# Kernel optimization log

Measured on AMD Instinct MI355X. Metric: run time of the kernel, lower is better.

Reference implementation:

```python
import jax, jax.numpy as jnp
import numpy as np

N = 50000          # nodes
E = 800000         # edges (before self-loops)
F_IN, F_HID, F_OUT = 128, 64, 64
NEG_SLOPE_ATT = 0.2   # GATConv internal leaky_relu
NEG_SLOPE_ACT = 0.01  # F.leaky_relu default between layers


def setup_inputs() -> dict:
    key = jax.random.key(0)
    ks = jax.random.split(key, 16)

    def glorot(k, shape):
        fan = float(sum(shape)) if len(shape) > 1 else float(shape[0])
        return jax.random.normal(k, shape, jnp.float32) * (2.0 / fan) ** 0.5

    return {
        "x": jax.random.normal(ks[0], (N, F_IN), jnp.float32),
        "edge_index": jax.random.randint(ks[1], (2, E), 0, N, dtype=jnp.int64),
        "W1": glorot(ks[2], (F_IN, F_HID)),
        "a_src1": glorot(ks[3], (F_HID,)),
        "a_dst1": glorot(ks[4], (F_HID,)),
        "b1": jnp.zeros((F_HID,), jnp.float32),
        "W2": glorot(ks[5], (F_HID, F_HID)),
        "a_src2": glorot(ks[6], (F_HID,)),
        "a_dst2": glorot(ks[7], (F_HID,)),
        "b2": jnp.zeros((F_HID,), jnp.float32),
        "W3": glorot(ks[8], (F_HID, F_OUT)),
        "a_src3": glorot(ks[9], (F_OUT,)),
        "a_dst3": glorot(ks[10], (F_OUT,)),
        "b3": jnp.zeros((F_OUT,), jnp.float32),
    }


def gat_conv(h, src, dst, W, a_src, a_dst, b):
    # Single-head PyG GATConv: project, per-edge scores, segment softmax over dst, scatter-add.
    z = h @ W                              # [N, C]
    e_src = z @ a_src                      # [N]
    e_dst = z @ a_dst                      # [N]
    e = jax.nn.leaky_relu(e_src[src] + e_dst[dst], NEG_SLOPE_ATT)  # [E']
    m = jax.ops.segment_max(e, dst, num_segments=N)
    ex = jnp.exp(e - m[dst])
    denom = jax.ops.segment_sum(ex, dst, num_segments=N)
    alpha = ex / (denom[dst] + 1e-16)      # segment softmax (PyG adds 1e-16)
    out = jax.ops.segment_sum(alpha[:, None] * z[src], dst, num_segments=N) + b
    return out, alpha


def reference(x, edge_index, W1, a_src1, a_dst1, b1, W2, a_src2, a_dst2, b2, W3, a_src3, a_dst3, b3):
    # add_self_loops=True (GATConv default): append (i, i) for every node
    loops = jnp.arange(N, dtype=edge_index.dtype)
    ei = jnp.concatenate([edge_index, jnp.stack([loops, loops])], axis=1)  # [2, E+N]
    src, dst = ei[0], ei[1]

    h = x
    alpha = None
    for (W, asr, ads, b) in ((W1, a_src1, a_dst1, b1),
                             (W2, a_src2, a_dst2, b2),
                             (W3, a_src3, a_dst3, b3)):
        h, alpha = gat_conv(h, src, dst, W, asr, ads, b)
        h = jax.nn.leaky_relu(h, NEG_SLOPE_ACT)
    return (h, ei, alpha)
```

## Files before the change

kernel.cpp:

```cpp
#include <hip/hip_runtime.h>
#include <hip/hip_bf16.h>
#include <hip/hip_fp8.h>

#define NN 50000
#define EE 800000
#define E2 850000
#define F_IN 128
#define F_HID 64
#define NTILE  ((NN + 63) / 64)
#define AGGB 2048

#define PNB 32
#define BCAP 32768
#define HBCH 512
#define CBB2 ((EE + HBCH - 1) / HBCH)
#define HCAP 40
#define SLICEB 64
#define BSPAN 1563

__device__ __forceinline__ unsigned char f32_to_fp8(float x) {
    __hip_fp8_e4m3 t(x);
    return t.__x;
}
__device__ __forceinline__ float fp8_to_f32(unsigned char b) {
    __hip_fp8_e4m3 t; t.__x = b;
    return (float)t;
}

#if defined(__has_builtin)
#  if __has_builtin(__builtin_amdgcn_cvt_f32_fp8)
#    define CVT_FP8(v, s) __builtin_amdgcn_cvt_f32_fp8((v), (s))
#  endif
#endif
#ifndef CVT_FP8
#  define CVT_FP8(v, s) fp8_to_f32(((v) >> (8 * (s))) & 255)
#endif

__global__ __launch_bounds__(256) void cast_bin(const int* __restrict__ ei,
                                                int* __restrict__ bin_cur,
                                                unsigned long long* __restrict__ bins,
                                                float* __restrict__ ei_out) {
    __shared__ unsigned long long buf[PNB * HCAP];
    __shared__ int wcnt[4][PNB];
    __shared__ int woff[4][PNB];
    __shared__ int tcn[PNB];
    __shared__ int gbase[PNB];
    __shared__ int pfx[PNB + 1];

    int tid = threadIdx.x, wv = tid >> 6;
    if (tid < 4 * PNB) ((int*)wcnt)[tid] = 0;
    __syncthreads();

    int e0 = blockIdx.x * HBCH;
    int nE = EE - e0; if (nE > HBCH) nE = HBCH;

    int sR[2], dR[2], bR[2], rk[2];
    bool act[2];
#pragma unroll
    for (int it = 0; it < 2; ++it) {
        int idx = it * 256 + tid;
        bool a = idx < nE;
        act[it] = a;
        int e = e0 + idx;
        int ss = 0, dd = 0, bb = 0, r = 0;
        if (a) {
            ss = ei[e]; dd = ei[EE + e];
            ei_out[e]      = (float)ss;
            ei_out[E2 + e] = (float)dd;
            bb = (int)(((long long)dd * PNB) / NN);
            r = atomicAdd(&wcnt[wv][bb], 1);
        }
        sR[it] = ss; dR[it] = dd; bR[it] = bb; rk[it] = r;
    }
    __syncthreads();

    if (tid < PNB) {
        int b = tid, r = 0;
        for (int w2 = 0; w2 < 4; ++w2) { int c = wcnt[w2][b]; woff[w2][b] = r; r += c; }
        int cl = (r > HCAP) ? HCAP : r;
        tcn[b] = cl;
        gbase[b] = cl ? atomicAdd(&bin_cur[b], cl) : 0;
    }
    __syncthreads();
    if (tid == 0) {
        int run = 0;
        for (int b = 0; b < PNB; ++b) { pfx[b] = run; run += tcn[b]; }
        pfx[PNB] = run;
    }
    __syncthreads();

#pragma unroll
    for (int it = 0; it < 2; ++it) {
        if (act[it]) {
            int b = bR[it];
            int idx = woff[wv][b] + rk[it];
            unsigned long long pk =
                ((unsigned long long)(unsigned)dR[it] << 32) | (unsigned)sR[it];
            if (idx < HCAP) buf[b * HCAP + idx] = pk;
            else {
                int p = atomicAdd(&bin_cur[b], 1);
                if (p < BCAP) bins[(size_t)b * BCAP + p] = pk;
            }
        }
    }
    __syncthreads();

    int total = pfx[PNB];
    for (int idx = tid; idx < total; idx += 256) {
        int lo = 0, hi = PNB;
        while (hi - lo > 1) { int mid = (lo + hi) >> 1; if (pfx[mid] <= idx) lo = mid; else hi = mid; }
        int b = lo, li = idx - pfx[b];
        int p = gbase[b] + li;
        if (p < BCAP) bins[(size_t)b * BCAP + p] = buf[b * HCAP + li];
    }
}

__global__ __launch_bounds__(1024) void count_scan(const int* __restrict__ bin_cur,
                                                   const unsigned long long* __restrict__ bins,
                                                   int* __restrict__ deg,
                                                   int* __restrict__ offs,
                                                   int* __restrict__ cursor,
                                                   int* __restrict__ src_sorted,
                                                   float* __restrict__ ei_out,
                                                   int* __restrict__ ticket,
                                                   int* __restrict__ flag,
                                                   int* __restrict__ bsum,
                                                   int* __restrict__ bbase) {
    __shared__ int cnt[BSPAN];
    __shared__ int wsm[16];
    __shared__ int totsh, lastsh, basesh;
    int t = threadIdx.x, lane = t & 63, wid = t >> 6;
    int b = blockIdx.x;
    int lo = (int)(((long long)b * NN + PNB - 1) / PNB);
    int hi = (int)(((long long)(b + 1) * NN + PNB - 1) / PNB);
    if (hi > NN) hi = NN;
    int span = hi - lo;
    for (int i = t; i < span; i += 1024) cnt[i] = 0;
    __syncthreads();
    int n = bin_cur[b]; if (n > BCAP) n = BCAP;
    const unsigned long long* bp = bins + (size_t)b * BCAP;
    for (int i = t; i < n; i += 1024)
        atomicAdd(&cnt[(int)(bp[i] >> 32) - lo], 1);
    __syncthreads();

    int i0 = 2 * t, i1 = 2 * t + 1;
    int v0 = (i0 < span) ? cnt[i0] + 1 : 0;
    int v1 = (i1 < span) ? cnt[i1] + 1 : 0;
    int s = v0 + v1, inc = s;
#pragma unroll
    for (int dd = 1; dd < 64; dd <<= 1) {
        int o = __shfl_up(inc, dd);
        if (lane >= dd) inc += o;
    }
    if (lane == 63) wsm[wid] = inc;
    __syncthreads();
    if (t < 16) {
        int v = wsm[t], ii = v;
#pragma unroll
        for (int dd = 1; dd < 16; dd <<= 1) {
            int o = __shfl_up(ii, dd);
            if (t >= dd) ii += o;
        }
        wsm[t] = ii - v;
        if (t == 15) totsh = ii;
    }
    __syncthreads();
    int eth = wsm[wid] + (inc - s);

    if (t == 0) {
        atomicExch(&bsum[b], totsh);
        __threadfence();
        lastsh = (atomicAdd(ticket, 1) == PNB - 1) ? 1 : 0;
    }
    __syncthreads();
    if (lastsh) {
        if (t == 0) {
            int run = 0;
            for (int q = 0; q < PNB; ++q) {
                int v = atomicAdd(&bsum[q], 0);
                atomicExch(&bbase[q], run);
                run += v;
            }
            __threadfence();
            atomicExch(flag, 1);
        }
    } else {
        if (t == 0) {
            while (atomicAdd(flag, 0) == 0) __builtin_amdgcn_s_sleep(8);
        }
    }
    __syncthreads();
    if (t == 0) basesh = atomicAdd(&bbase[b], 0);
    __syncthreads();
    int base = basesh;

    if (i0 < span) {
        int d = lo + i0, ex = base + eth;
        offs[d] = ex; cursor[d] = ex + 1; deg[d] = v0 - 1;
        src_sorted[ex] = d;
        ei_out[EE + d]      = (float)d;
        ei_out[E2 + EE + d] = (float)d;
    }
    if (i1 < span) {
        int d = lo + i1, ex = base + eth + v0;
        offs[d] = ex; cursor[d] = ex + 1; deg[d] = v1 - 1;
        src_sorted[ex] = d;
        ei_out[EE + d]      = (float)d;
        ei_out[E2 + EE + d] = (float)d;
    }
}

__global__ __launch_bounds__(256) void scatter_bins(const int* __restrict__ bin_cur,
                                                    const unsigned long long* __restrict__ bins,
                                                    int* __restrict__ cursor,
                                                    int* __restrict__ src_sorted) {
    int b = blockIdx.x & (PNB - 1);
    int slice = blockIdx.x >> 5;
    int cnt = bin_cur[b];
    if (cnt > BCAP) cnt = BCAP;
    const unsigned long long* bp = bins + (size_t)b * BCAP;
    for (int i = slice * 256 + threadIdx.x; i < cnt; i += SLICEB * 256) {
        unsigned long long v = bp[i];
        int d = (int)(v >> 32);
        int s = (int)(v & 0xffffffffu);
        int pos = atomicAdd(&cursor[d], 1);
        src_sorted[pos] = s;
    }
}

template <int K>
__global__ __launch_bounds__(256) void gemm_tile(const float* __restrict__ h,
                                                 const float* __restrict__ W,
                                                 const float* __restrict__ a_src,
                                                 const float* __restrict__ a_dst,
                                                 unsigned char* __restrict__ z8,
                                                 float* __restrict__ es,
                                                 float* __restrict__ ed) {
    constexpr int LDA = K + 4;
    __shared__ float Alds[64 * LDA];
    __shared__ float Blds[K * 64];

    int tid = threadIdx.x;
    int base = blockIdx.x * 64;

    {
        constexpr int F4R = K / 4;
        for (int t = tid; t < 64 * F4R; t += 256) {
            int r = t / F4R;
            int c4 = t % F4R;
            int gr = base + r;
            if (gr >= NN) gr = NN - 1;
            float4 v = *(const float4*)(h + (size_t)gr * K + c4 * 4);
            *(float4*)(&Alds[r * LDA + c4 * 4]) = v;
        }
    }
    for (int t = tid; t < K * 16; t += 256) {
        float4 v = *(const float4*)(W + t * 4);
        *(float4*)(&Blds[t * 4]) = v;
    }
    __syncthreads();

    int tx = tid & 15;
    int ty = tid >> 4;

    float acc[4][4] = {};
#pragma unroll 4
    for (int k = 0; k < K; k += 4) {
        float4 a[4], b[4];
#pragma unroll
        for (int i = 0; i < 4; ++i)
            a[i] = *(const float4*)(&Alds[(4 * ty + i) * LDA + k]);
#pragma unroll
        for (int kk = 0; kk < 4; ++kk)
            b[kk] = *(const float4*)(&Blds[(k + kk) * 64 + 4 * tx]);
#pragma unroll
        for (int i = 0; i < 4; ++i) {
            acc[i][0] = fmaf(a[i].x, b[0].x, acc[i][0]);
            acc[i][1] = fmaf(a[i].x, b[0].y, acc[i][1]);
            acc[i][2] = fmaf(a[i].x, b[0].z, acc[i][2]);
            acc[i][3] = fmaf(a[i].x, b[0].w, acc[i][3]);
            acc[i][0] = fmaf(a[i].y, b[1].x, acc[i][0]);
            acc[i][1] = fmaf(a[i].y, b[1].y, acc[i][1]);
            acc[i][2] = fmaf(a[i].y, b[1].z, acc[i][2]);
            acc[i][3] = fmaf(a[i].y, b[1].w, acc[i][3]);
            acc[i][0] = fmaf(a[i].z, b[2].x, acc[i][0]);
            acc[i][1] = fmaf(a[i].z, b[2].y, acc[i][1]);
            acc[i][2] = fmaf(a[i].z, b[2].z, acc[i][2]);
            acc[i][3] = fmaf(a[i].z, b[2].w, acc[i][3]);
            acc[i][0] = fmaf(a[i].w, b[3].x, acc[i][0]);
            acc[i][1] = fmaf(a[i].w, b[3].y, acc[i][1]);
            acc[i][2] = fmaf(a[i].w, b[3].z, acc[i][2]);
            acc[i][3] = fmaf(a[i].w, b[3].w, acc[i][3]);
        }
    }

    float4 as4 = *(const float4*)(a_src + 4 * tx);
    float4 ad4 = *(const float4*)(a_dst + 4 * tx);
    float ps[4], pd[4];
#pragma unroll
    for (int i = 0; i < 4; ++i) {
        int gr = base + 4 * ty + i;
        if (gr < NN) {
            unsigned int pk = (unsigned int)f32_to_fp8(acc[i][0])
                            | ((unsigned int)f32_to_fp8(acc[i][1]) << 8)
                            | ((unsigned int)f32_to_fp8(acc[i][2]) << 16)
                            | ((unsigned int)f32_to_fp8(acc[i][3]) << 24);
            *(unsigned int*)(&z8[(size_t)gr * 64 + 4 * tx]) = pk;
        }
        ps[i] = acc[i][0] * as4.x + acc[i][1] * as4.y + acc[i][2] * as4.z + acc[i][3] * as4.w;
        pd[i] = acc[i][0] * ad4.x + acc[i][1] * ad4.y + acc[i][2] * ad4.z + acc[i][3] * ad4.w;
    }
#pragma unroll
    for (int d = 1; d < 16; d <<= 1) {
#pragma unroll
        for (int i = 0; i < 4; ++i) {
            ps[i] += __shfl_xor(ps[i], d);
            pd[i] += __shfl_xor(pd[i], d);
        }
    }
    if (tx == 0) {
#pragma unroll
        for (int i = 0; i < 4; ++i) {
            int gr = base + 4 * ty + i;
            if (gr < NN) { es[gr] = ps[i]; ed[gr] = pd[i]; }
        }
    }
}

__global__ __launch_bounds__(256) void aggregate(const int* __restrict__ offs,
                                                 const int* __restrict__ deg,
                                                 const int* __restrict__ src_sorted,
                                                 const float* __restrict__ es,
                                                 const float* __restrict__ ed,
                                                 const unsigned char* __restrict__ z8,
                                                 const float* __restrict__ bias,
                                                 float* __restrict__ hout,
                                                 float* __restrict__ denom_out) {
    __shared__ unsigned long long swl[4][64];
    int tid = threadIdx.x;
    int lane = tid & 63;
    int wslot = tid >> 6;
    int wave = blockIdx.x * 4 + wslot;
    const int NW = AGGB * 4;

    int sub  = lane >> 4;
    int fgrp = (lane & 15) * 4;
    const unsigned char* zp = z8 + fgrp;
    float4 bi4 = *(const float4*)(bias + fgrp);

    int n = wave;
    if (n >= NN) return;
    n = __builtin_amdgcn_readfirstlane(n);
    int off = offs[n];
    int dg = deg[n] + 1;
    float edn = ed[n];
    int sv = src_sorted[off + ((lane < dg) ? lane : 0)];
    float ese = es[sv];

    while (true) {
        int n2 = n + NW;
        bool more = (n2 < NN);
        int off2 = 0, dg2 = 0; float edn2 = 0.f;
        if (more) {
            n2 = __builtin_amdgcn_readfirstlane(n2);
            off2 = offs[n2]; dg2 = deg[n2] + 1; edn2 = ed[n2];
        }

        float dsum = 0.f;
        float a0 = 0.f, a1 = 0.f, a2 = 0.f, a3 = 0.f;
        for (int b0 = 0; b0 < dg; b0 += 64) {
            int bl = dg - b0; if (bl > 64) bl = 64;
            int svb; float esv;
            if (b0 == 0) { svb = sv; esv = ese; }
            else {
                svb = src_sorted[off + b0 + ((lane < bl) ? lane : 0)];
                esv = es[svb];
            }
            float e = esv + edn;
            e = (e > 0.f) ? e : 0.2f * e;
            float w = (lane < bl) ? __expf(e) : 0.f;
            dsum += w;

            swl[wslot][lane] = ((unsigned long long)__float_as_uint(w) << 32)
                             | (unsigned)(svb << 6);

            int ng = (bl + 3) >> 2;
            int j = 0;
            for (; j + 4 <= ng; j += 4) {
                int i0 = 4 * j + sub;
                unsigned long long p0 = swl[wslot][i0];
                unsigned long long p1 = swl[wslot][i0 + 4];
                unsigned long long p2 = swl[wslot][i0 + 8];
                unsigned long long p3 = swl[wslot][i0 + 12];
                unsigned int v0 = *(const unsigned int*)(zp + (unsigned)p0);
                unsigned int v1 = *(const unsigned int*)(zp + (unsigned)p1);
                unsigned int v2 = *(const unsigned int*)(zp + (unsigned)p2);
                unsigned int v3 = *(const unsigned int*)(zp + (unsigned)p3);
                float w0 = __uint_as_float((unsigned)(p0 >> 32));
                float w1 = __uint_as_float((unsigned)(p1 >> 32));
                float w2 = __uint_as_float((unsigned)(p2 >> 32));
                float w3 = __uint_as_float((unsigned)(p3 >> 32));
                a0 = fmaf(w0, CVT_FP8(v0, 0), a0);
                a1 = fmaf(w0, CVT_FP8(v0, 1), a1);
                a2 = fmaf(w0, CVT_FP8(v0, 2), a2);
                a3 = fmaf(w0, CVT_FP8(v0, 3), a3);
                a0 = fmaf(w1, CVT_FP8(v1, 0), a0);
                a1 = fmaf(w1, CVT_FP8(v1, 1), a1);
                a2 = fmaf(w1, CVT_FP8(v1, 2), a2);
                a3 = fmaf(w1, CVT_FP8(v1, 3), a3);
                a0 = fmaf(w2, CVT_FP8(v2, 0), a0);
                a1 = fmaf(w2, CVT_FP8(v2, 1), a1);
                a2 = fmaf(w2, CVT_FP8(v2, 2), a2);
                a3 = fmaf(w2, CVT_FP8(v2, 3), a3);
                a0 = fmaf(w3, CVT_FP8(v3, 0), a0);
                a1 = fmaf(w3, CVT_FP8(v3, 1), a1);
                a2 = fmaf(w3, CVT_FP8(v3, 2), a2);
                a3 = fmaf(w3, CVT_FP8(v3, 3), a3);
            }
            for (; j < ng; ++j) {
                int i0 = 4 * j + sub;
                unsigned long long p0 = swl[wslot][i0];
                unsigned int v0 = *(const unsigned int*)(zp + (unsigned)p0);
                float w0 = __uint_as_float((unsigned)(p0 >> 32));
                a0 = fmaf(w0, CVT_FP8(v0, 0), a0);
                a1 = fmaf(w0, CVT_FP8(v0, 1), a1);
                a2 = fmaf(w0, CVT_FP8(v0, 2), a2);
                a3 = fmaf(w0, CVT_FP8(v0, 3), a3);
            }
        }

        int sv2 = 0;
        if (more) sv2 = src_sorted[off2 + ((lane < dg2) ? lane : 0)];

        a0 += __shfl_xor(a0, 16); a1 += __shfl_xor(a1, 16);
        a2 += __shfl_xor(a2, 16); a3 += __shfl_xor(a3, 16);
        a0 += __shfl_xor(a0, 32); a1 += __shfl_xor(a1, 32);
        a2 += __shfl_xor(a2, 32); a3 += __shfl_xor(a3, 32);
#pragma unroll
        for (int d = 32; d; d >>= 1) dsum += __shfl_xor(dsum, d);

        float ese2 = 0.f;
        if (more) ese2 = es[sv2];

        float inv = 1.f / (dsum + 1e-16f);
        if (lane < 16) {
            float4 o;
            o.x = a0 * inv + bi4.x;
            o.y = a1 * inv + bi4.y;
            o.z = a2 * inv + bi4.z;
            o.w = a3 * inv + bi4.w;
            o.x = (o.x > 0.f) ? o.x : 0.01f * o.x;
            o.y = (o.y > 0.f) ? o.y : 0.01f * o.y;
            o.z = (o.z > 0.f) ? o.z : 0.01f * o.z;
            o.w = (o.w > 0.f) ? o.w : 0.01f * o.w;
            *(float4*)(hout + (size_t)n * 64 + fgrp) = o;
        }
        if (lane == 0) denom_out[n] = dsum;

        if (!more) break;
        n = n2; off = off2; dg = dg2; edn = edn2; sv = sv2; ese = ese2;
    }
}

__global__ __launch_bounds__(256) void alpha_kernel(const int* __restrict__ ei,
                                                    const float* __restrict__ es,
                                                    const float* __restrict__ ed,
                                                    const float* __restrict__ denom,
                                                    float* __restrict__ alpha_out) {
    int e = blockIdx.x * 256 + threadIdx.x;
    if (e >= E2) return;
    int s, d;
    if (e < EE) { s = ei[e]; d = ei[EE + e]; }
    else        { s = d = e - EE; }
    float x = es[s] + ed[d];
    x = (x > 0.f) ? x : 0.2f * x;
    alpha_out[e] = __expf(x) / (denom[d] + 1e-16f);
}

extern "C" void kernel_launch(void* const* d_in, const int* in_sizes, int n_in,
                              void* d_out, int out_size, void* d_ws, size_t ws_size,
                              hipStream_t stream) {
    const float* x   = (const float*)d_in[0];
    const int*   ei  = (const int*)d_in[1];
    const float* W1  = (const float*)d_in[2];
    const float* as1 = (const float*)d_in[3];
    const float* ad1 = (const float*)d_in[4];
    const float* b1  = (const float*)d_in[5];
    const float* W2  = (const float*)d_in[6];
    const float* as2 = (const float*)d_in[7];
    const float* ad2 = (const float*)d_in[8];
    const float* b2  = (const float*)d_in[9];
    const float* W3  = (const float*)d_in[10];
    const float* as3 = (const float*)d_in[11];
    const float* ad3 = (const float*)d_in[12];
    const float* b3  = (const float*)d_in[13];

    float* out       = (float*)d_out;
    float* h_out     = out;
    float* ei_out    = out + (size_t)NN * 64;
    float* alpha_out = ei_out + 2 * (size_t)E2;

    char* w = (char*)d_ws;
    auto carve = [&](size_t bytes) {
        void* p = (void*)w;
        w += (bytes + 255) & ~size_t(255);
        return p;
    };
    float* h1  = (float*)carve((size_t)NN * 64 * 4);
    float* h2  = (float*)carve((size_t)NN * 64 * 4);
    unsigned char* z8 = (unsigned char*)carve((size_t)NN * 64);
    float* es  = (float*)carve((size_t)NN * 4);
    float* ed  = (float*)carve((size_t)NN * 4);
    float* denom = (float*)carve((size_t)NN * 4);
    int* deg        = (int*)carve(((size_t)NN + 160) * 4);
    int* ticket     = deg + NN;
    int* flag       = deg + NN + 1;
    int* bin_cur    = deg + NN + 2;
    int* bsum       = deg + NN + 34;
    int* bbase      = deg + NN + 66;
    int* offs       = (int*)carve((size_t)NN * 4);
    int* cursor     = (int*)carve((size_t)NN * 4);
    int* src_sorted = (int*)carve((size_t)E2 * 4);
    unsigned long long* bins = (unsigned long long*)carve((size_t)PNB * BCAP * 8);

    const int EB = (E2 + 255) / 256;

    hipMemsetAsync(deg + NN, 0, 160 * 4, stream);
    cast_bin<<<CBB2, 256, 0, stream>>>(ei, bin_cur, bins, ei_out);
    count_scan<<<PNB, 1024, 0, stream>>>(bin_cur, bins, deg, offs, cursor,
                                         src_sorted, ei_out, ticket, flag, bsum, bbase);
    scatter_bins<<<PNB * SLICEB, 256, 0, stream>>>(bin_cur, bins, cursor, src_sorted);

    gemm_tile<F_IN><<<NTILE, 256, 0, stream>>>(x, W1, as1, ad1, z8, es, ed);
    aggregate<<<AGGB, 256, 0, stream>>>(offs, deg, src_sorted, es, ed, z8, b1, h1, denom);
    gemm_tile<F_HID><<<NTILE, 256, 0, stream>>>(h1, W2, as2, ad2, z8, es, ed);
    aggregate<<<AGGB, 256, 0, stream>>>(offs, deg, src_sorted, es, ed, z8, b2, h2, denom);
    gemm_tile<F_HID><<<NTILE, 256, 0, stream>>>(h2, W3, as3, ad3, z8, es, ed);
    aggregate<<<AGGB, 256, 0, stream>>>(offs, deg, src_sorted, es, ed, z8, b3, h_out, denom);
    alpha_kernel<<<EB, 256, 0, stream>>>(ei, es, ed, denom, alpha_out);
}
```

Before: 290.0 us.

## Software-pipeline aggregate gathers across nodes with double-buffered LDS staging

Restructures the per-wave aggregation loop into a deeper software pipeline. For nodes with degree at most 32, the fp8 feature gathers for the current node are issued before the previous node's gathered values are consumed, and a double-buffered LDS slot keeps the two nodes' weights apart. Index prefetch now runs two nodes ahead. This aims to hide gather latency behind the FMA work, at the cost of more live registers and extra control flow, which may reduce occupancy.

```diff
diff --git a/kernel.cpp b/kernel.cpp
--- a/kernel.cpp
+++ b/kernel.cpp
@@ -327,6 +327,42 @@
     }
 }
 
+#define CONS(PAR, G, V)                                                   \
+  { unsigned long long q_ = swl[ws][PAR][(G) * 4 + sub];                  \
+    float wg_ = __uint_as_float((unsigned)(q_ >> 32));                    \
+    a0 = fmaf(wg_, CVT_FP8(V, 0), a0);                                    \
+    a1 = fmaf(wg_, CVT_FP8(V, 1), a1);                                    \
+    a2 = fmaf(wg_, CVT_FP8(V, 2), a2);                                    \
+    a3 = fmaf(wg_, CVT_FP8(V, 3), a3); }
+
+#define EPILOGUE(NODE, DS)                                                \
+  { a0 += __shfl_xor(a0, 16); a1 += __shfl_xor(a1, 16);                   \
+    a2 += __shfl_xor(a2, 16); a3 += __shfl_xor(a3, 16);                   \
+    a0 += __shfl_xor(a0, 32); a1 += __shfl_xor(a1, 32);                   \
+    a2 += __shfl_xor(a2, 32); a3 += __shfl_xor(a3, 32);                   \
+    _Pragma("unroll")                                                     \
+    for (int d_ = 32; d_; d_ >>= 1) DS += __shfl_xor(DS, d_);             \
+    float inv_ = 1.f / (DS + 1e-16f);                                     \
+    if (lane < 16) {                                                      \
+        float4 o_;                                                        \
+        o_.x = a0 * inv_ + bi4.x; o_.y = a1 * inv_ + bi4.y;               \
+        o_.z = a2 * inv_ + bi4.z; o_.w = a3 * inv_ + bi4.w;               \
+        o_.x = (o_.x > 0.f) ? o_.x : 0.01f * o_.x;                        \
+        o_.y = (o_.y > 0.f) ? o_.y : 0.01f * o_.y;                        \
+        o_.z = (o_.z > 0.f) ? o_.z : 0.01f * o_.z;                        \
+        o_.w = (o_.w > 0.f) ? o_.w : 0.01f * o_.w;                        \
+        *(float4*)(hout + (size_t)(NODE) * 64 + fgrp) = o_;               \
+    }                                                                     \
+    if (lane == 0) denom_out[NODE] = DS; }
+
+#define CONSUME_P()                                                       \
+  { float a0 = 0, a1 = 0, a2 = 0, a3 = 0;                                 \
+    CONS(parP, 0, vp0) CONS(parP, 1, vp1) CONS(parP, 2, vp2)              \
+    CONS(parP, 3, vp3) CONS(parP, 4, vp4) CONS(parP, 5, vp5)              \
+    CONS(parP, 6, vp6) CONS(parP, 7, vp7)                                 \
+    float dsum = wlP;                                                     \
+    EPILOGUE(nP, dsum) }
+
 __global__ __launch_bounds__(256) void aggregate(const int* __restrict__ offs,
                                                  const int* __restrict__ deg,
                                                  const int* __restrict__ src_sorted,
@@ -336,11 +372,11 @@
                                                  const float* __restrict__ bias,
                                                  float* __restrict__ hout,
                                                  float* __restrict__ denom_out) {
-    __shared__ unsigned long long swl[4][64];
+    __shared__ unsigned long long swl[4][2][64];
     int tid = threadIdx.x;
     int lane = tid & 63;
-    int wslot = tid >> 6;
-    int wave = blockIdx.x * 4 + wslot;
+    int ws = tid >> 6;
+    int wave = blockIdx.x * 4 + ws;
     const int NW = AGGB * 4;
 
     int sub  = lane >> 4;
@@ -348,118 +384,110 @@
     const unsigned char* zp = z8 + fgrp;
     float4 bi4 = *(const float4*)(bias + fgrp);
 
-    int n = wave;
-    if (n >= NN) return;
-    n = __builtin_amdgcn_readfirstlane(n);
-    int off = offs[n];
-    int dg = deg[n] + 1;
-    float edn = ed[n];
-    int sv = src_sorted[off + ((lane < dg) ? lane : 0)];
-    float ese = es[sv];
-
-    while (true) {
-        int n2 = n + NW;
-        bool more = (n2 < NN);
-        int off2 = 0, dg2 = 0; float edn2 = 0.f;
-        if (more) {
-            n2 = __builtin_amdgcn_readfirstlane(n2);
-            off2 = offs[n2]; dg2 = deg[n2] + 1; edn2 = ed[n2];
-        }
-
-        float dsum = 0.f;
-        float a0 = 0.f, a1 = 0.f, a2 = 0.f, a3 = 0.f;
-        for (int b0 = 0; b0 < dg; b0 += 64) {
-            int bl = dg - b0; if (bl > 64) bl = 64;
-            int svb; float esv;
-            if (b0 == 0) { svb = sv; esv = ese; }
-            else {
-                svb = src_sorted[off + b0 + ((lane < bl) ? lane : 0)];
-                esv = es[svb];
+    if (wave >= NN) return;
+
+    int nC = __builtin_amdgcn_readfirstlane(wave);
+    int offC = offs[nC]; int dgC = deg[nC] + 1; float ednC = ed[nC];
+    int svC = src_sorted[offC + ((lane < dgC) ? lane : 0)];
+    float eseC = es[svC];
+
+    int nN = nC + NW; bool hasN = (nN < NN);
+    int offN = 0, dgN = 0; float ednN = 0.f; int svN = 0;
+    if (hasN) {
+        nN = __builtin_amdgcn_readfirstlane(nN);
+        offN = offs[nN]; dgN = deg[nN] + 1; ednN = ed[nN];
+        svN = src_sorted[offN + ((lane < dgN) ? lane : 0)];
+    }
+
+    bool hasP = false;
+    int nP = 0, parP = 0;
+    float wlP = 0.f;
+    unsigned vp0=0,vp1=0,vp2=0,vp3=0,vp4=0,vp5=0,vp6=0,vp7=0;
+
+    int par = 0;
+    bool hasC = true;
+
+    while (hasC) {
+        float eseN = 0.f;
+        if (hasN) eseN = es[svN];
+
+        int nX = hasN ? nN + NW : NN;
+        bool hasX = (nX < NN);
+        int offX = 0, dgX = 0; float ednX = 0.f;
+        if (hasX) {
+            nX = __builtin_amdgcn_readfirstlane(nX);
+            offX = offs[nX]; dgX = deg[nX] + 1; ednX = ed[nX];
+        }
+
+        bool fastC = (dgC <= 32);
+        float wlC = 0.f;
+        unsigned va0=0,va1=0,va2=0,va3=0,va4=0,va5=0,va6=0,va7=0;
+        if (fastC) {
+            float e_ = eseC + ednC;
+            e_ = (e_ > 0.f) ? e_ : 0.2f * e_;
+            wlC = (lane < dgC) ? __expf(e_) : 0.f;
+            swl[ws][par][lane] =
+                ((unsigned long long)__float_as_uint(wlC) << 32) | (unsigned)(svC << 6);
+            unsigned long long q;
+            q = swl[ws][par][ 0 + sub]; va0 = *(const unsigned int*)(zp + (unsigned)q);
+            q = swl[ws][par][ 4 + sub]; va1 = *(const unsigned int*)(zp + (unsigned)q);
+            q = swl[ws][par][ 8 + sub]; va2 = *(const unsigned int*)(zp + (unsigned)q);
+            q = swl[ws][par][12 + sub]; va3 = *(const unsigned int*)(zp + (unsigned)q);
+            q = swl[ws][par][16 + sub]; va4 = *(const unsigned int*)(zp + (unsigned)q);
+            q = swl[ws][par][20 + sub]; va5 = *(const unsigned int*)(zp + (unsigned)q);
+            q = swl[ws][par][24 + sub]; va6 = *(const unsigned int*)(zp + (unsigned)q);
+            q = swl[ws][par][28 + sub]; va7 = *(const unsigned int*)(zp + (unsigned)q);
+        }
+
+        if (hasP) { CONSUME_P() }
+
+        if (!fastC) {
+            float a0 = 0, a1 = 0, a2 = 0, a3 = 0;
+            float dsum = 0.f;
+            for (int b0 = 0; b0 < dgC; b0 += 64) {
+                int bl = dgC - b0; if (bl > 64) bl = 64;
+                int svb; float esv;
+                if (b0 == 0) { svb = svC; esv = eseC; }
+                else {
+                    svb = src_sorted[offC + b0 + ((lane < bl) ? lane : 0)];
+                    esv = es[svb];
+                }
+                float e = esv + ednC;
+                e = (e > 0.f) ? e : 0.2f * e;
+                float w = (lane < bl) ? __expf(e) : 0.f;
+                dsum += w;
+                swl[ws][par][lane] =
+                    ((unsigned long long)__float_as_uint(w) << 32) | (unsigned)(svb << 6);
+                int ng = (bl + 3) >> 2;
+                for (int g = 0; g < ng; ++g) {
+                    unsigned long long q = swl[ws][par][g * 4 + sub];
+                    unsigned v = *(const unsigned int*)(zp + (unsigned)q);
+                    float wg = __uint_as_float((unsigned)(q >> 32));
+                    a0 = fmaf(wg, CVT_FP8(v, 0), a0);
+                    a1 = fmaf(wg, CVT_FP8(v, 1), a1);
+                    a2 = fmaf(wg, CVT_FP8(v, 2), a2);
+                    a3 = fmaf(wg, CVT_FP8(v, 3), a3);
+                }
             }
-            float e = esv + edn;
-            e = (e > 0.f) ? e : 0.2f * e;
-            float w = (lane < bl) ? __expf(e) : 0.f;
-            dsum += w;
-
-            swl[wslot][lane] = ((unsigned long long)__float_as_uint(w) << 32)
-                             | (unsigned)(svb << 6);
-
-            int ng = (bl + 3) >> 2;
-            int j = 0;
-            for (; j + 4 <= ng; j += 4) {
-                int i0 = 4 * j + sub;
-                unsigned long long p0 = swl[wslot][i0];
-                unsigned long long p1 = swl[wslot][i0 + 4];
-                unsigned long long p2 = swl[wslot][i0 + 8];
-                unsigned long long p3 = swl[wslot][i0 + 12];
-                unsigned int v0 = *(const unsigned int*)(zp + (unsigned)p0);
-                unsigned int v1 = *(const unsigned int*)(zp + (unsigned)p1);
-                unsigned int v2 = *(const unsigned int*)(zp + (unsigned)p2);
-                unsigned int v3 = *(const unsigned int*)(zp + (unsigned)p3);
-                float w0 = __uint_as_float((unsigned)(p0 >> 32));
-                float w1 = __uint_as_float((unsigned)(p1 >> 32));
-                float w2 = __uint_as_float((unsigned)(p2 >> 32));
-                float w3 = __uint_as_float((unsigned)(p3 >> 32));
-                a0 = fmaf(w0, CVT_FP8(v0, 0), a0);
-                a1 = fmaf(w0, CVT_FP8(v0, 1), a1);
-                a2 = fmaf(w0, CVT_FP8(v0, 2), a2);
-                a3 = fmaf(w0, CVT_FP8(v0, 3), a3);
-                a0 = fmaf(w1, CVT_FP8(v1, 0), a0);
-                a1 = fmaf(w1, CVT_FP8(v1, 1), a1);
-                a2 = fmaf(w1, CVT_FP8(v1, 2), a2);
-                a3 = fmaf(w1, CVT_FP8(v1, 3), a3);
-                a0 = fmaf(w2, CVT_FP8(v2, 0), a0);
-                a1 = fmaf(w2, CVT_FP8(v2, 1), a1);
-                a2 = fmaf(w2, CVT_FP8(v2, 2), a2);
-                a3 = fmaf(w2, CVT_FP8(v2, 3), a3);
-                a0 = fmaf(w3, CVT_FP8(v3, 0), a0);
-                a1 = fmaf(w3, CVT_FP8(v3, 1), a1);
-                a2 = fmaf(w3, CVT_FP8(v3, 2), a2);
-                a3 = fmaf(w3, CVT_FP8(v3, 3), a3);
-            }
-            for (; j < ng; ++j) {
-                int i0 = 4 * j + sub;
-                unsigned long long p0 = swl[wslot][i0];
-                unsigned int v0 = *(const unsigned int*)(zp + (unsigned)p0);
-                float w0 = __uint_as_float((unsigned)(p0 >> 32));
-                a0 = fmaf(w0, CVT_FP8(v0, 0), a0);
-                a1 = fmaf(w0, CVT_FP8(v0, 1), a1);
-                a2 = fmaf(w0, CVT_FP8(v0, 2), a2);
-                a3 = fmaf(w0, CVT_FP8(v0, 3), a3);
-            }
-        }
-
-        int sv2 = 0;
-        if (more) sv2 = src_sorted[off2 + ((lane < dg2) ? lane : 0)];
-
-        a0 += __shfl_xor(a0, 16); a1 += __shfl_xor(a1, 16);
-        a2 += __shfl_xor(a2, 16); a3 += __shfl_xor(a3, 16);
-        a0 += __shfl_xor(a0, 32); a1 += __shfl_xor(a1, 32);
-        a2 += __shfl_xor(a2, 32); a3 += __shfl_xor(a3, 32);
-#pragma unroll
-        for (int d = 32; d; d >>= 1) dsum += __shfl_xor(dsum, d);
-
-        float ese2 = 0.f;
-        if (more) ese2 = es[sv2];
-
-        float inv = 1.f / (dsum + 1e-16f);
-        if (lane < 16) {
-            float4 o;
-            o.x = a0 * inv + bi4.x;
-            o.y = a1 * inv + bi4.y;
-            o.z = a2 * inv + bi4.z;
-            o.w = a3 * inv + bi4.w;
-            o.x = (o.x > 0.f) ? o.x : 0.01f * o.x;
-            o.y = (o.y > 0.f) ? o.y : 0.01f * o.y;
-            o.z = (o.z > 0.f) ? o.z : 0.01f * o.z;
-            o.w = (o.w > 0.f) ? o.w : 0.01f * o.w;
-            *(float4*)(hout + (size_t)n * 64 + fgrp) = o;
-        }
-        if (lane == 0) denom_out[n] = dsum;
-
-        if (!more) break;
-        n = n2; off = off2; dg = dg2; edn = edn2; sv = sv2; ese = ese2;
-    }
+            EPILOGUE(nC, dsum)
+            hasP = false;
+        } else {
+            hasP = true; nP = nC; parP = par;
+            wlP = wlC;
+            vp0=va0; vp1=va1; vp2=va2; vp3=va3; vp4=va4; vp5=va5; vp6=va6; vp7=va7;
+        }
+        par ^= 1;
+
+        int svX = 0;
+        if (hasX) svX = src_sorted[offX + ((lane < dgX) ? lane : 0)];
+
+        hasC = hasN;
+        nC = nN; offC = offN; dgC = dgN; ednC = ednN; svC = svN; eseC = eseN;
+        hasN = hasX;
+        nN = nX; offN = offX; dgN = dgX; ednN = ednX; svN = svX;
+    }
+
+    if (hasP) { CONSUME_P() }
 }
 
 __global__ __launch_bounds__(256) void alpha_kernel(const int* __restrict__ ei,
```

Measured after the change: 313.5 us. 1.08x slower.
